# Kernel tuning notes

Hardware: AMD Instinct MI355X
Metric: run time of the kernel (lower is better)

Reference implementation:

```python
import jax, jax.numpy as jnp
import numpy as np

ITERS = 5          # iter_node_counts
N, M, Z, E = 68, 46, 384, 368   # base VNs, base CNs, lifting size, total base edges
LLR_CLIP = 20.0    # allowed_llr_range.abs
BIG = 1e9


def setup_inputs() -> dict:
    key = jax.random.key(0)
    k1, k2, k3 = jax.random.split(key, 3)
    B = 64
    # channel LLRs, realistic AWGN-ish magnitudes
    xa = jax.random.normal(k1, (B, N, Z), dtype=jnp.float32) * 4.0
    edge_vn = jax.random.randint(k2, (E,), 0, N, dtype=jnp.int32)
    # regular check degree 8 so every check has >=2 edges (valid min-sum extrinsics)
    edge_cn = (jnp.arange(E, dtype=jnp.int32) % M)
    edge_shift = jax.random.randint(k3, (E,), 0, Z, dtype=jnp.int32)  # circulant shifts
    cn_weight = jnp.ones((ITERS,), dtype=jnp.float32)  # scalar CN weight per iteration
    return {"xa": xa, "cn_weight": cn_weight, "edge_vn": edge_vn,
            "edge_cn": edge_cn, "edge_shift": edge_shift}


def _qms5(x):
    # QMS q_bit=5 quantizer with straight-through estimator
    q = jnp.clip(jnp.round(x * 2.0) / 2.0, -7.5, 7.5)
    xc = jnp.clip(x, -7.5, 7.5)
    return xc + jax.lax.stop_gradient(q - xc)


def _decode(xa, cn_weight, edge_vn, edge_cn, edge_shift):
    B = xa.shape[0]
    xa_in = jnp.transpose(xa, (0, 2, 1))  # [B, Z, N]
    z = jnp.arange(Z)
    # lifting (Lift_Matrix1): cyclic shift each edge's Z copies; unlift is inverse
    idx_lift = ((z[:, None] - edge_shift[None, :]) % Z)[None]    # [1, Z, E]
    idx_unlift = ((z[:, None] + edge_shift[None, :]) % Z)[None]  # [1, Z, E]
    c2v = jnp.zeros((B, Z, E), dtype=xa.dtype)  # prev_llr (CN->VN messages)
    ch = jnp.moveaxis(xa_in, 2, 0)  # [N, B, Z]
    outs = []
    for it in range(ITERS):
        # --- odd layer (VN update): W_skipconn2even + W_odd2even ---
        vn_sum = jax.ops.segment_sum(jnp.moveaxis(c2v, 2, 0), edge_vn, num_segments=N)  # [N,B,Z]
        tot = ch + vn_sum                                  # total belief per VN
        v2c = jnp.moveaxis(tot[edge_vn], 0, 2) - c2v       # extrinsic, [B,Z,E]
        v2c = jnp.clip(v2c, -LLR_CLIP, LLR_CLIP)           # allowed_llr_range
        v2c = jnp.take_along_axis(v2c, idx_lift, axis=1)   # Lift_Matrix1
        # --- even layer (CN update, min-sum): W_even2odd ---
        vE = jnp.moveaxis(v2c, 2, 0)                       # [E, B, Z]
        mag = jnp.abs(vE)
        neg = (vE < 0).astype(jnp.int32)
        cnt = jax.ops.segment_sum(neg, edge_cn, num_segments=M)      # [M,B,Z]
        csign = (1 - 2 * (cnt % 2)).astype(vE.dtype)                 # sign product per CN
        min1 = jax.ops.segment_min(mag, edge_cn, num_segments=M)
        is_min = mag == min1[edge_cn]
        min2 = jax.ops.segment_min(jnp.where(is_min, BIG, mag), edge_cn, num_segments=M)
        ext_min = jnp.where(is_min, min2[edge_cn], min1[edge_cn])
        own_sign = jnp.where(vE < 0, -1.0, 1.0).astype(vE.dtype)
        ext = csign[edge_cn] * own_sign * ext_min          # extrinsic min-sum message
        ext = _qms5(cn_weight[it] * ext)                   # learned CN weight + QMS quantize
        c2v = jnp.moveaxis(ext, 0, 2)                      # [B,Z,E]
        c2v = jnp.take_along_axis(c2v, idx_unlift, axis=1) # Lift_Matrix2
        # --- output marginalization: W_output ---
        out = xa_in + jnp.moveaxis(
            jax.ops.segment_sum(jnp.moveaxis(c2v, 2, 0), edge_vn, num_segments=N), 0, 2)
        outs.append(out)
    return jnp.stack(outs)  # [ITERS, B, Z, N]


def reference(xa, cn_weight, edge_vn, edge_cn, edge_shift):
    return _decode(xa, cn_weight, edge_vn, edge_cn, edge_shift)
```

## Files before the change

kernel.cpp:

```cpp
#include <hip/hip_runtime.h>


#define ITERS 5
#define Nn 68
#define Mm 46
#define Zz 384
#define Ee 368
#define Bb 64
#define Kk 8
#define PADD 24
#define BIGF 1e9f

#define ROWB (Bb*Zz)
#define TOT_ELEMS (Nn*Bb*Zz)
#define C2V_BYTES ((Ee+1)*ROWB)
#define TOT_OFF   0
#define C2V_OFF   (TOT_ELEMS*4)
#define DEG_OFF   (C2V_OFF + C2V_BYTES)
#define VOFF_OFF  (DEG_OFF + 384)

__global__ __launch_bounds__(256) void init_kernel(
    const int* __restrict__ edge_vn, signed char* __restrict__ c2v,
    int* __restrict__ vn_deg, int* __restrict__ voff)
{
    if (blockIdx.x == 0) {
        int4* p = (int4*)(c2v + (size_t)Ee * ROWB);
        for (int i = threadIdx.x; i < ROWB / 16; i += 256)
            p[i] = make_int4(0, 0, 0, 0);
    } else {
        __shared__ int sev[Ee];
        for (int t = threadIdx.x; t < Ee; t += 256) sev[t] = edge_vn[t];
        __syncthreads();
        int n = threadIdx.x;
        if (n < Nn) {
            int d = 0;
            for (int e = 0; e < Ee; e++)
                if (sev[e] == n && d < PADD) voff[n * PADD + (d++)] = e * ROWB;
            vn_deg[n] = d;
            for (int j = d; j < PADD; j++) voff[n * PADD + j] = Ee * ROWB;
        }
    }
}

__device__ __forceinline__ void minsum_store(
    const float v[Kk], const int off[Kk], float m1, unsigned sflip,
    float w, signed char* __restrict__ c2v)
{
    float m2 = BIGF;
    #pragma unroll
    for (int k = 0; k < Kk; k++) {
        float mag = fabsf(v[k]);
        if (mag != m1) m2 = fminf(m2, mag);
    }
    #pragma unroll
    for (int k = 0; k < Kk; k++) {
        float mag  = fabsf(v[k]);
        float emin = (mag == m1) ? m2 : m1;
        unsigned neg = sflip ^ ((v[k] < 0.0f) ? 1u : 0u);
        float ext = neg ? -emin : emin;
        float r = rintf(w * ext * 2.0f);
        r = fminf(15.0f, fmaxf(-15.0f, r));
        c2v[off[k]] = (signed char)(int)r;
    }
}

__global__ __launch_bounds__(384) void cn0_kernel(
    const float* __restrict__ xa,
    signed char* __restrict__ c2v,
    const int* __restrict__ edge_vn, const int* __restrict__ edge_shift,
    const float* __restrict__ cn_weight)
{
    const int cn = blockIdx.x;
    const int b  = blockIdx.y;
    const int zc = threadIdx.x;
    const float w = cn_weight[0];

    float v[Kk];
    int   off[Kk];
    float m1 = BIGF;
    unsigned sflip = 0u;

    #pragma unroll
    for (int k = 0; k < Kk; k++) {
        int e  = cn + k * Mm;
        int sh = edge_shift[e];
        int n  = edge_vn[e];
        int z  = zc - sh;
        z += (z >> 31) & Zz;
        off[k] = e * ROWB + b * Zz + z;
        float x = xa[(b * Nn + n) * Zz + z];
        x = fminf(20.0f, fmaxf(-20.0f, x));
        v[k] = x;
        if (x < 0.0f) sflip ^= 1u;
        m1 = fminf(m1, fabsf(x));
    }
    minsum_store(v, off, m1, sflip, w, c2v);
}

__global__ __launch_bounds__(384) void cn_kernel(
    const float* __restrict__ tot, signed char* __restrict__ c2v,
    const int* __restrict__ edge_vn, const int* __restrict__ edge_shift,
    const float* __restrict__ cn_weight, int it)
{
    const int cn = blockIdx.x;
    const int b  = blockIdx.y;
    const int zc = threadIdx.x;
    const float w = cn_weight[it];

    float v[Kk];
    int   off[Kk];
    float m1 = BIGF;
    unsigned sflip = 0u;

    #pragma unroll
    for (int k = 0; k < Kk; k++) {
        int e  = cn + k * Mm;
        int sh = edge_shift[e];
        int n  = edge_vn[e];
        int z  = zc - sh;
        z += (z >> 31) & Zz;
        int o = e * ROWB + b * Zz + z;
        off[k] = o;
        float t = tot[(n * Bb + b) * Zz + z];
        float c = 0.5f * (float)c2v[o];
        float x = t - c;
        x = fminf(20.0f, fmaxf(-20.0f, x));
        v[k] = x;
        if (x < 0.0f) sflip ^= 1u;
        m1 = fminf(m1, fabsf(x));
    }
    minsum_store(v, off, m1, sflip, w, c2v);
}

__global__ __launch_bounds__(256) void vn_kernel(
    const float* __restrict__ xa, const signed char* __restrict__ c2v,
    float* __restrict__ tot, float* __restrict__ out,
    const int* __restrict__ vn_deg, const int* __restrict__ voff,
    int write_tot)
{
    __shared__ float tile[17][65];
    const int b  = blockIdx.x;
    const int z0 = blockIdx.y * 64;
    const int n0 = blockIdx.z * 17;
    const int wave = threadIdx.x >> 6;
    const int lane = threadIdx.x & 63;
    const int z = z0 + lane;
    const int bz = b * Zz + z;

    for (int i = wave; i < 17; i += 4) {
        int n = __builtin_amdgcn_readfirstlane(n0 + i);
        int d = vn_deg[n];
        const int* vo = voff + n * PADD;
        int acc = 0;
        #pragma unroll
        for (int j = 0; j < 8; j++) acc += (int)c2v[vo[j] + bz];
        if (d > 8) {
            #pragma unroll
            for (int j = 8; j < 16; j++) acc += (int)c2v[vo[j] + bz];
        }
        if (d > 16) {
            #pragma unroll
            for (int j = 16; j < PADD; j++) acc += (int)c2v[vo[j] + bz];
        }
        float s = xa[(size_t)(b * Nn + n) * Zz + z] + 0.5f * (float)acc;
        if (write_tot) tot[(n * Bb + b) * Zz + z] = s;
        tile[i][lane] = s;
    }
    __syncthreads();

    float* dst = out + ((size_t)b * Zz + z0) * Nn + n0;
    for (int idx = threadIdx.x; idx < 17 * 64; idx += 256) {
        int zz = idx / 17;
        int nn = idx - zz * 17;
        dst[(size_t)zz * Nn + nn] = tile[nn][zz];
    }
}

extern "C" void kernel_launch(void* const* d_in, const int* in_sizes, int n_in,
                              void* d_out, int out_size, void* d_ws, size_t ws_size,
                              hipStream_t stream) {
    const float* xa        = (const float*)d_in[0];
    const float* cn_weight = (const float*)d_in[1];
    const int*   edge_vn   = (const int*)d_in[2];
    const int*   edge_shift= (const int*)d_in[4];
    float* out = (float*)d_out;

    char* ws = (char*)d_ws;
    float*       tot    = (float*)(ws + TOT_OFF);
    signed char* c2v    = (signed char*)(ws + C2V_OFF);
    int*         vn_deg = (int*)(ws + DEG_OFF);
    int*         voff   = (int*)(ws + VOFF_OFF);

    init_kernel<<<2, 256, 0, stream>>>(edge_vn, c2v, vn_deg, voff);

    for (int it = 0; it < ITERS; it++) {
        if (it == 0)
            cn0_kernel<<<dim3(Mm, Bb), 384, 0, stream>>>(xa, c2v, edge_vn,
                                                         edge_shift, cn_weight);
        else
            cn_kernel<<<dim3(Mm, Bb), 384, 0, stream>>>(tot, c2v, edge_vn,
                                                        edge_shift, cn_weight, it);
        vn_kernel<<<dim3(Bb, Zz / 64, 4), 256, 0, stream>>>(
            xa, c2v, tot, out + (size_t)it * Bb * Zz * Nn,
            vn_deg, voff, (it != ITERS - 1) ? 1 : 0);
    }
}
```

Before: 188.9 us.

## Bias-encode c2v bytes and sum four z lanes per dword in VN kernel

Stores c2v messages as unsigned bytes offset by 32, so the VN kernel can load four consecutive z values as one dword and accumulate them with packed SWAR adds. It also sorts VNs by degree in the init kernel so neighbouring threads take the same degree branches, and stages the offset tables in shared memory. The shared-memory transpose for the output is removed; each thread now writes strided scalar stores. The intent is fewer byte loads and less branch divergence, at the cost of less coalesced output writes and possibly unaligned dword loads of c2v.

```diff
diff --git a/kernel.cpp b/kernel.cpp
--- a/kernel.cpp
+++ b/kernel.cpp
@@ -16,19 +16,23 @@
 #define C2V_BYTES ((Ee+1)*ROWB)
 #define TOT_OFF   0
 #define C2V_OFF   (TOT_ELEMS*4)
-#define DEG_OFF   (C2V_OFF + C2V_BYTES)
-#define VOFF_OFF  (DEG_OFF + 384)
+#define PN_OFF    (C2V_OFF + C2V_BYTES)
+#define PD_OFF    (PN_OFF + Nn*4)
+#define PVOFF_OFF (PD_OFF + Nn*4)
 
 __global__ __launch_bounds__(256) void init_kernel(
-    const int* __restrict__ edge_vn, signed char* __restrict__ c2v,
-    int* __restrict__ vn_deg, int* __restrict__ voff)
+    const int* __restrict__ edge_vn, unsigned char* __restrict__ c2v,
+    int* __restrict__ g_pn, int* __restrict__ g_pdeg, int* __restrict__ g_pvoff)
 {
     if (blockIdx.x == 0) {
         int4* p = (int4*)(c2v + (size_t)Ee * ROWB);
-        for (int i = threadIdx.x; i < ROWB / 16; i += 256)
-            p[i] = make_int4(0, 0, 0, 0);
+        const int4 v = make_int4(0x20202020, 0x20202020, 0x20202020, 0x20202020);
+        for (int i = threadIdx.x; i < ROWB / 16; i += 256) p[i] = v;
     } else {
         __shared__ int sev[Ee];
+        __shared__ int deg[Nn];
+        __shared__ int voff[Nn * PADD];
+        __shared__ int perm[Nn];
         for (int t = threadIdx.x; t < Ee; t += 256) sev[t] = edge_vn[t];
         __syncthreads();
         int n = threadIdx.x;
@@ -36,15 +40,32 @@
             int d = 0;
             for (int e = 0; e < Ee; e++)
                 if (sev[e] == n && d < PADD) voff[n * PADD + (d++)] = e * ROWB;
-            vn_deg[n] = d;
+            deg[n] = d;
             for (int j = d; j < PADD; j++) voff[n * PADD + j] = Ee * ROWB;
+        }
+        __syncthreads();
+        if (threadIdx.x == 0) {
+            for (int i = 0; i < Nn; i++) perm[i] = i;
+            for (int i = 1; i < Nn; i++) {
+                int p = perm[i], key = deg[p], j = i - 1;
+                while (j >= 0 && deg[perm[j]] > key) { perm[j + 1] = perm[j]; j--; }
+                perm[j + 1] = p;
+            }
+        }
+        __syncthreads();
+        if (threadIdx.x < Nn) {
+            int src = perm[threadIdx.x];
+            g_pn[threadIdx.x]   = src;
+            g_pdeg[threadIdx.x] = deg[src];
+            for (int j = 0; j < PADD; j++)
+                g_pvoff[threadIdx.x * PADD + j] = voff[src * PADD + j];
         }
     }
 }
 
 __device__ __forceinline__ void minsum_store(
     const float v[Kk], const int off[Kk], float m1, unsigned sflip,
-    float w, signed char* __restrict__ c2v)
+    float w, unsigned char* __restrict__ c2v)
 {
     float m2 = BIGF;
     #pragma unroll
@@ -60,13 +81,13 @@
         float ext = neg ? -emin : emin;
         float r = rintf(w * ext * 2.0f);
         r = fminf(15.0f, fmaxf(-15.0f, r));
-        c2v[off[k]] = (signed char)(int)r;
+        c2v[off[k]] = (unsigned char)((int)r + 32);
     }
 }
 
 __global__ __launch_bounds__(384) void cn0_kernel(
     const float* __restrict__ xa,
-    signed char* __restrict__ c2v,
+    unsigned char* __restrict__ c2v,
     const int* __restrict__ edge_vn, const int* __restrict__ edge_shift,
     const float* __restrict__ cn_weight)
 {
@@ -75,10 +96,8 @@
     const int zc = threadIdx.x;
     const float w = cn_weight[0];
 
-    float v[Kk];
-    int   off[Kk];
-    float m1 = BIGF;
-    unsigned sflip = 0u;
+    float v[Kk]; int off[Kk];
+    float m1 = BIGF; unsigned sflip = 0u;
 
     #pragma unroll
     for (int k = 0; k < Kk; k++) {
@@ -98,7 +117,7 @@
 }
 
 __global__ __launch_bounds__(384) void cn_kernel(
-    const float* __restrict__ tot, signed char* __restrict__ c2v,
+    const float* __restrict__ tot, unsigned char* __restrict__ c2v,
     const int* __restrict__ edge_vn, const int* __restrict__ edge_shift,
     const float* __restrict__ cn_weight, int it)
 {
@@ -107,10 +126,8 @@
     const int zc = threadIdx.x;
     const float w = cn_weight[it];
 
-    float v[Kk];
-    int   off[Kk];
-    float m1 = BIGF;
-    unsigned sflip = 0u;
+    float v[Kk]; int off[Kk];
+    float m1 = BIGF; unsigned sflip = 0u;
 
     #pragma unroll
     for (int k = 0; k < Kk; k++) {
@@ -122,8 +139,7 @@
         int o = e * ROWB + b * Zz + z;
         off[k] = o;
         float t = tot[(n * Bb + b) * Zz + z];
-        float c = 0.5f * (float)c2v[o];
-        float x = t - c;
+        float x = t - 0.5f * (float)((int)c2v[o] - 32);
         x = fminf(20.0f, fmaxf(-20.0f, x));
         v[k] = x;
         if (x < 0.0f) sflip ^= 1u;
@@ -133,46 +149,65 @@
 }
 
 __global__ __launch_bounds__(256) void vn_kernel(
-    const float* __restrict__ xa, const signed char* __restrict__ c2v,
+    const float* __restrict__ xa, const unsigned char* __restrict__ c2v,
     float* __restrict__ tot, float* __restrict__ out,
-    const int* __restrict__ vn_deg, const int* __restrict__ voff,
-    int write_tot)
-{
-    __shared__ float tile[17][65];
+    const int* __restrict__ g_pn, const int* __restrict__ g_pdeg,
+    const int* __restrict__ g_pvoff, int write_tot)
+{
+    __shared__ int s_voff[Nn * PADD];
+    __shared__ int s_pn[Nn], s_pd[Nn];
     const int b  = blockIdx.x;
-    const int z0 = blockIdx.y * 64;
-    const int n0 = blockIdx.z * 17;
-    const int wave = threadIdx.x >> 6;
-    const int lane = threadIdx.x & 63;
-    const int z = z0 + lane;
-    const int bz = b * Zz + z;
-
-    for (int i = wave; i < 17; i += 4) {
-        int n = __builtin_amdgcn_readfirstlane(n0 + i);
-        int d = vn_deg[n];
-        const int* vo = voff + n * PADD;
-        int acc = 0;
+    const int z0 = blockIdx.y * 32;
+    for (int t = threadIdx.x; t < Nn * PADD; t += 256) s_voff[t] = g_pvoff[t];
+    if (threadIdx.x < Nn) {
+        s_pn[threadIdx.x] = g_pn[threadIdx.x];
+        s_pd[threadIdx.x] = g_pdeg[threadIdx.x];
+    }
+    __syncthreads();
+
+    for (int m = threadIdx.x; m < Nn * 8; m += 256) {
+        int i = m >> 3, s = m & 7;
+        int z = z0 + 4 * s;
+        int n = s_pd ? s_pn[i] : 0;
+        int d = s_pd[i];
+        const int* vo = s_voff + i * PADD;
+        int base = b * Zz + z;
+        unsigned ae = 0u, ao = 0u;
         #pragma unroll
-        for (int j = 0; j < 8; j++) acc += (int)c2v[vo[j] + bz];
+        for (int j = 0; j < 8; j++) {
+            unsigned u = *(const unsigned*)(c2v + (vo[j] + base));
+            ae += u & 0x00FF00FFu;
+            ao += (u >> 8) & 0x00FF00FFu;
+        }
+        int L = 8;
         if (d > 8) {
+            L = 16;
             #pragma unroll
-            for (int j = 8; j < 16; j++) acc += (int)c2v[vo[j] + bz];
-        }
-        if (d > 16) {
-            #pragma unroll
-            for (int j = 16; j < PADD; j++) acc += (int)c2v[vo[j] + bz];
-        }
-        float s = xa[(size_t)(b * Nn + n) * Zz + z] + 0.5f * (float)acc;
-        if (write_tot) tot[(n * Bb + b) * Zz + z] = s;
-        tile[i][lane] = s;
-    }
-    __syncthreads();
-
-    float* dst = out + ((size_t)b * Zz + z0) * Nn + n0;
-    for (int idx = threadIdx.x; idx < 17 * 64; idx += 256) {
-        int zz = idx / 17;
-        int nn = idx - zz * 17;
-        dst[(size_t)zz * Nn + nn] = tile[nn][zz];
+            for (int j = 8; j < 16; j++) {
+                unsigned u = *(const unsigned*)(c2v + (vo[j] + base));
+                ae += u & 0x00FF00FFu;
+                ao += (u >> 8) & 0x00FF00FFu;
+            }
+            if (d > 16) {
+                L = 24;
+                #pragma unroll
+                for (int j = 16; j < PADD; j++) {
+                    unsigned u = *(const unsigned*)(c2v + (vo[j] + base));
+                    ae += u & 0x00FF00FFu;
+                    ao += (u >> 8) & 0x00FF00FFu;
+                }
+            }
+        }
+        int bias = 32 * L;
+        float4 x = *(const float4*)(xa + (size_t)(b * Nn + n) * Zz + z);
+        float s0 = x.x + 0.5f * (float)((int)(ae & 0xFFFFu) - bias);
+        float s1 = x.y + 0.5f * (float)((int)(ao & 0xFFFFu) - bias);
+        float s2 = x.z + 0.5f * (float)((int)(ae >> 16) - bias);
+        float s3 = x.w + 0.5f * (float)((int)(ao >> 16) - bias);
+        if (write_tot)
+            *(float4*)(tot + (n * Bb + b) * Zz + z) = make_float4(s0, s1, s2, s3);
+        float* op = out + ((size_t)b * Zz + z) * Nn + n;
+        op[0] = s0; op[Nn] = s1; op[2 * Nn] = s2; op[3 * Nn] = s3;
     }
 }
 
@@ -186,12 +221,13 @@
     float* out = (float*)d_out;
 
     char* ws = (char*)d_ws;
-    float*       tot    = (float*)(ws + TOT_OFF);
-    signed char* c2v    = (signed char*)(ws + C2V_OFF);
-    int*         vn_deg = (int*)(ws + DEG_OFF);
-    int*         voff   = (int*)(ws + VOFF_OFF);
-
-    init_kernel<<<2, 256, 0, stream>>>(edge_vn, c2v, vn_deg, voff);
+    float*         tot     = (float*)(ws + TOT_OFF);
+    unsigned char* c2v     = (unsigned char*)(ws + C2V_OFF);
+    int*           g_pn    = (int*)(ws + PN_OFF);
+    int*           g_pdeg  = (int*)(ws + PD_OFF);
+    int*           g_pvoff = (int*)(ws + PVOFF_OFF);
+
+    init_kernel<<<2, 256, 0, stream>>>(edge_vn, c2v, g_pn, g_pdeg, g_pvoff);
 
     for (int it = 0; it < ITERS; it++) {
         if (it == 0)
@@ -200,8 +236,8 @@
         else
             cn_kernel<<<dim3(Mm, Bb), 384, 0, stream>>>(tot, c2v, edge_vn,
                                                         edge_shift, cn_weight, it);
-        vn_kernel<<<dim3(Bb, Zz / 64, 4), 256, 0, stream>>>(
+        vn_kernel<<<dim3(Bb, Zz / 32), 256, 0, stream>>>(
             xa, c2v, tot, out + (size_t)it * Bb * Zz * Nn,
-            vn_deg, voff, (it != ITERS - 1) ? 1 : 0);
-    }
-}
+            g_pn, g_pdeg, g_pvoff, (it != ITERS - 1) ? 1 : 0);
+    }
+}
```

New measurement: 294.8 us. 1.56x slower.
